# Optimization experiments

Measured on AMD Instinct MI355X. Metric: run time of the kernel, lower is better.

The kernel has to match this reference:

```python
import jax, jax.numpy as jnp
import numpy as np

NP_, NC_, E_, F_, D_, O_ = 50000, 100000, 600000, 69, 128, 2


def _embed(x, shift, scale, w1, b1, w2, b2):
    # PreNormLayer (shift+scale) -> Linear -> ReLU -> Linear -> ReLU
    x = (x + shift) * scale
    return jax.nn.relu(jax.nn.relu(x @ w1 + b1) @ w2 + b2)


def _biconv(left, src, dst, right, wl, bl, wr, sf, wf, bf, sp, wo1, bo1, wo2, bo2):
    # message: final( left_mod(right[dst]) + right_mod(left[src]) ), mean-scatter to dst
    pre = (right[dst] @ wl + bl) + left[src] @ wr            # [E, D]
    msg = jax.nn.relu(pre * sf) @ wf + bf                    # [E, D]
    n = right.shape[0]
    sums = jax.ops.segment_sum(msg, dst, num_segments=n)     # [N_right, D]
    cnt = jax.ops.segment_sum(jnp.ones((dst.shape[0], 1), msg.dtype), dst, num_segments=n)
    agg = sums / jnp.maximum(cnt, 1.0)
    h = jnp.concatenate([agg * sp, right], axis=-1)          # [N_right, 2D]
    return jax.nn.relu(h @ wo1 + bo1) @ wo2 + bo2


def setup_inputs():
    key = jax.random.key(0)
    ks = jax.random.split(key, 40)
    it = iter(range(4, 40))
    def nw(shape):
        return (jax.random.normal(ks[next(it)], shape, dtype=jnp.float32) * 0.05)
    inp = {}
    inp['pivot_features'] = jax.random.normal(ks[0], (NP_, F_), dtype=jnp.float32)
    inp['children_features'] = jax.random.normal(ks[1], (NC_, F_), dtype=jnp.float32)
    src = jax.random.randint(ks[2], (E_,), 0, NP_, dtype=jnp.int32)
    dst = jax.random.randint(ks[3], (E_,), 0, NC_, dtype=jnp.int32)
    inp['edge_indices'] = jnp.stack([src, dst], axis=0)
    # pivot / children embedding MLPs (PreNorm buffers at init values)
    for p in ('pe', 'ce'):
        inp[p + '_shift'] = jnp.zeros((F_,), jnp.float32)
        inp[p + '_scale'] = jnp.ones((F_,), jnp.float32)
        inp[p + '_w1'] = nw((F_, D_)); inp[p + '_b1'] = jnp.zeros((D_,), jnp.float32)
        inp[p + '_w2'] = nw((D_, D_)); inp[p + '_b2'] = jnp.zeros((D_,), jnp.float32)
    # two bipartite conv layers
    for p in ('vc', 'cv'):
        inp[p + '_wl'] = nw((D_, D_)); inp[p + '_bl'] = jnp.zeros((D_,), jnp.float32)
        inp[p + '_wr'] = nw((D_, D_))
        inp[p + '_sf'] = jnp.ones((1,), jnp.float32)   # PreNormLayer(1, shift=False) scale
        inp[p + '_wf'] = nw((D_, D_)); inp[p + '_bf'] = jnp.zeros((D_,), jnp.float32)
        inp[p + '_sp'] = jnp.ones((1,), jnp.float32)   # post_conv PreNormLayer scale
        inp[p + '_wo1'] = nw((2 * D_, D_)); inp[p + '_bo1'] = jnp.zeros((D_,), jnp.float32)
        inp[p + '_wo2'] = nw((D_, D_)); inp[p + '_bo2'] = jnp.zeros((D_,), jnp.float32)
    inp['out_w1'] = nw((D_, D_)); inp['out_b1'] = jnp.zeros((D_,), jnp.float32)
    inp['out_w2'] = nw((D_, O_)); inp['out_b2'] = jnp.zeros((O_,), jnp.float32)
    return inp


def reference(pivot_features, children_features, edge_indices,
              pe_shift, pe_scale, pe_w1, pe_b1, pe_w2, pe_b2,
              ce_shift, ce_scale, ce_w1, ce_b1, ce_w2, ce_b2,
              vc_wl, vc_bl, vc_wr, vc_sf, vc_wf, vc_bf, vc_sp, vc_wo1, vc_bo1, vc_wo2, vc_bo2,
              cv_wl, cv_bl, cv_wr, cv_sf, cv_wf, cv_bf, cv_sp, cv_wo1, cv_bo1, cv_wo2, cv_bo2,
              out_w1, out_b1, out_w2, out_b2):
    pv = _embed(pivot_features, pe_shift, pe_scale, pe_w1, pe_b1, pe_w2, pe_b2)
    ch = _embed(children_features, ce_shift, ce_scale, ce_w1, ce_b1, ce_w2, ce_b2)
    src, dst = edge_indices[0], edge_indices[1]
    # conv_v_to_c: left=pivot, right=children, aggregate to children
    ch = _biconv(pv, src, dst, ch, vc_wl, vc_bl, vc_wr, vc_sf, vc_wf, vc_bf, vc_sp,
                 vc_wo1, vc_bo1, vc_wo2, vc_bo2)
    # conv_c_to_v with reversed edges: left=children, right=pivot, aggregate to pivot
    pv = _biconv(ch, dst, src, pv, cv_wl, cv_bl, cv_wr, cv_sf, cv_wf, cv_bf, cv_sp,
                 cv_wo1, cv_bo1, cv_wo2, cv_bo2)
    return jax.nn.sigmoid(jax.nn.relu(pv @ out_w1 + out_b1) @ out_w2 + out_b2)
```

## Files before the change

### kernel.cpp

```cpp
#include <hip/hip_runtime.h>
#include <math.h>


typedef unsigned short u16;
typedef __attribute__((ext_vector_type(8))) short s8v;
typedef __attribute__((ext_vector_type(4))) float f4v;

__device__ __forceinline__ float bf2f(u16 u) {
    unsigned x = ((unsigned)u) << 16;
    return __builtin_bit_cast(float, x);
}
__device__ __forceinline__ u16 f2bf(float f) {
    unsigned x = __builtin_bit_cast(unsigned, f);
    unsigned r = x + 0x7fffu + ((x >> 16) & 1u);
    return (u16)(r >> 16);
}
__device__ __forceinline__ unsigned pk2(float a, float b) {
    return (unsigned)f2bf(a) | ((unsigned)f2bf(b) << 16);
}
__device__ __forceinline__ void unpack8(uint4 u, float* f) {
    f[0] = bf2f((u16)(u.x & 0xffff)); f[1] = bf2f((u16)(u.x >> 16));
    f[2] = bf2f((u16)(u.y & 0xffff)); f[3] = bf2f((u16)(u.y >> 16));
    f[4] = bf2f((u16)(u.z & 0xffff)); f[5] = bf2f((u16)(u.z >> 16));
    f[6] = bf2f((u16)(u.w & 0xffff)); f[7] = bf2f((u16)(u.w >> 16));
}

struct SmEnt { const float* A; const float* B; const float* s; };
struct SmPack { SmEnt e[4]; };

__global__ __launch_bounds__(256) void smallmm(SmPack p, float* __restrict__ out)
{
    int t = blockIdx.x * 256 + threadIdx.x;
    int m = t >> 14;
    int o = t & 16383;
    int i = o >> 7, j = o & 127;
    SmEnt en = p.e[m];
    float acc = 0.f;
#pragma unroll 4
    for (int k = 0; k < 128; ++k) acc += en.A[i * 128 + k] * en.B[k * 128 + j];
    if (en.s) acc *= *en.s;
    out[(size_t)m * 16384 + o] = acc;
}

__global__ void vecpre(
    const float* vc_bf, const float* vc_wo1, const float* vc_sp,
    const float* cv_bf, const float* cv_wo1, const float* cv_sp,
    const float* vc_bo2, const float* cv_wr,
    const float* cv_bo2, const float* out_w1, const float* out_b1,
    float* __restrict__ vout)
{
    int j = threadIdx.x;
    if (j >= 128) return;
    float a0 = 0.f, a1 = 0.f, a2 = 0.f, a3 = 0.f;
    for (int k = 0; k < 128; ++k) {
        a0 += vc_bf[k] * vc_wo1[k * 128 + j];
        a1 += cv_bf[k] * cv_wo1[k * 128 + j];
        a2 += vc_bo2[k] * cv_wr[k * 128 + j];
        a3 += cv_bo2[k] * out_w1[k * 128 + j];
    }
    vout[j] = a0 * (*vc_sp);
    vout[128 + j] = a1 * (*cv_sp);
    vout[256 + j] = a2;
    vout[384 + j] = a3 + out_b1[j];
}

struct WEnt { const float* src; int Ksrc; int Kdst; };
struct WPack { WEnt e[14]; };

__global__ __launch_bounds__(256) void wconvert(WPack p, u16* __restrict__ wt)
{
    int t = blockIdx.x * 256 + threadIdx.x;
    int m = t >> 15;
    int i = t & 32767;
    WEnt en = p.e[m];
    if (i >= (en.Kdst << 7)) return;
    int k = i >> 7, col = i & 127;
    float v = (k < en.Ksrc) ? en.src[k * 128 + col] : 0.f;
    wt[(size_t)m * 32768 + (size_t)col * en.Kdst + k] = f2bf(v);
}

__global__ __launch_bounds__(256) void featconv2(
    const float* __restrict__ pv, const float* __restrict__ ch,
    const float* __restrict__ psh, const float* __restrict__ psc,
    const float* __restrict__ csh, const float* __restrict__ csc,
    u16* __restrict__ y, long NPr, long total, int F)
{
    for (long i = (long)blockIdx.x * 256 + threadIdx.x; i < total;
         i += (long)gridDim.x * 256) {
        int cc = (int)(i % 96);
        long r = i / 96;
        const float *x, *sh, *sc;
        long row;
        if (r < NPr) { x = pv; sh = psh; sc = psc; row = r; }
        else { x = ch; sh = csh; sc = csc; row = r - NPr; }
        float v = 0.f;
        if (cc < F) {
            v = x[row * F + cc];
            v = (v + sh[cc]) * sc[cc];
        }
        y[i] = f2bf(v);
    }
}

template <int KS1, bool HASA2, bool RELU, bool GATE>
__global__ __launch_bounds__(256) void gemm_rb(
    const u16* __restrict__ A1, const u16* __restrict__ A2,
    const u16* __restrict__ WT1,
    const u16* __restrict__ WT2,
    const float* __restrict__ bias0,
    const float* __restrict__ bias1,
    const float* __restrict__ gate,
    u16* __restrict__ out, int M)
{
    constexpr int K1 = KS1 * 32;
    constexpr bool PF = !HASA2;
    constexpr int AS = KS1 + (HASA2 ? 4 : 0);
    const int lane = threadIdx.x & 63;
    const int c = lane & 15;
    const int kg = lane >> 4;
    const int wid = blockIdx.x * 4 + (threadIdx.x >> 6);
    const int ws = gridDim.x * 4;
    const int items = M >> 4;

    const u16* wbase = WT1 + (size_t)c * K1 + kg * 8;
    s8v bp[KS1][8];
#pragma unroll
    for (int ks = 0; ks < KS1; ++ks)
#pragma unroll
        for (int nt = 0; nt < 8; ++nt)
            bp[ks][nt] = *(const s8v*)(wbase + ((size_t)nt * 16) * K1 + ks * 32);

    const u16* wbase2 = HASA2 ? (WT2 + (size_t)c * 128 + kg * 8) : nullptr;

    f4v bq[8];
#pragma unroll
    for (int nt = 0; nt < 8; ++nt)
        bq[nt] = bias0 ? *(const f4v*)(bias0 + nt * 16 + kg * 4)
                       : (f4v){0.f, 0.f, 0.f, 0.f};

    auto lda = [&](s8v* a, int item) {
        const u16* ap = A1 + (size_t)((item << 4) + c) * K1 + kg * 8;
#pragma unroll
        for (int ks = 0; ks < KS1; ++ks) a[ks] = *(const s8v*)(ap + ks * 32);
        if (HASA2) {
            const u16* ap2 = A2 + (size_t)((item << 4) + c) * 128 + kg * 8;
#pragma unroll
            for (int ks = 0; ks < 4; ++ks) a[KS1 + ks] = *(const s8v*)(ap2 + ks * 32);
        }
    };

    s8v a[AS], an[AS], a2[AS];
    int item = wid;
    if (item < items) lda(a, item);
    if (PF && item + ws < items) lda(an, item + ws);
    while (item < items) {
        const int i2 = item + 2 * ws;
        if (PF && i2 < items) lda(a2, i2);

        f4v acc[8];
#pragma unroll
        for (int nt = 0; nt < 8; ++nt) acc[nt] = (f4v){0.f, 0.f, 0.f, 0.f};
#pragma unroll
        for (int ks = 0; ks < KS1; ++ks)
#pragma unroll
            for (int nt = 0; nt < 8; ++nt)
                acc[nt] = __builtin_amdgcn_mfma_f32_16x16x32_bf16(bp[ks][nt], a[ks], acc[nt], 0, 0, 0);
        if (HASA2) {
#pragma unroll
            for (int ks = 0; ks < 4; ++ks)
#pragma unroll
                for (int nt = 0; nt < 8; ++nt) {
                    s8v b = *(const s8v*)(wbase2 + ((size_t)nt * 16) * 128 + ks * 32);
                    acc[nt] = __builtin_amdgcn_mfma_f32_16x16x32_bf16(b, a[KS1 + ks], acc[nt], 0, 0, 0);
                }
        }

        const int r0 = item << 4;
        const float g = GATE ? (gate[r0 + c] > 0.f ? 1.f : 0.f) : 0.f;
        u16* op = out + (size_t)(r0 + c) * 128 + kg * 4;
#pragma unroll
        for (int nt = 0; nt < 8; ++nt) {
            float v0 = acc[nt][0] + bq[nt][0];
            float v1 = acc[nt][1] + bq[nt][1];
            float v2 = acc[nt][2] + bq[nt][2];
            float v3 = acc[nt][3] + bq[nt][3];
            if (GATE && bias1) {
                f4v b1q = *(const f4v*)(bias1 + nt * 16 + kg * 4);
                v0 += g * b1q[0]; v1 += g * b1q[1];
                v2 += g * b1q[2]; v3 += g * b1q[3];
            }
            if (RELU) {
                v0 = fmaxf(v0, 0.f); v1 = fmaxf(v1, 0.f);
                v2 = fmaxf(v2, 0.f); v3 = fmaxf(v3, 0.f);
            }
            uint2 pkv;
            pkv.x = pk2(v0, v1);
            pkv.y = pk2(v2, v3);
            *(uint2*)(op + nt * 16) = pkv;
        }

        if (PF) {
#pragma unroll
            for (int ks = 0; ks < AS; ++ks) { a[ks] = an[ks]; an[ks] = a2[ks]; }
        } else if (item + ws < items) {
            lda(a, item + ws);
        }
        item += ws;
    }
}

struct GJob { const u16* A1; const u16* WT1; const float* bias0; u16* out; int M; };
struct GJobs3 { GJob j[3]; };

template <int KS1, bool RELU>
__global__ __launch_bounds__(256) void gemm_multi(GJobs3 jobs)
{
    constexpr int K1 = KS1 * 32;
    const GJob jb = jobs.j[blockIdx.y];
    const u16* __restrict__ A1 = jb.A1;
    const float* __restrict__ bias0 = jb.bias0;
    u16* __restrict__ out = jb.out;
    const int lane = threadIdx.x & 63;
    const int c = lane & 15;
    const int kg = lane >> 4;
    const int wid = blockIdx.x * 4 + (threadIdx.x >> 6);
    const int ws = gridDim.x * 4;
    const int items = jb.M >> 4;

    const u16* wbase = jb.WT1 + (size_t)c * K1 + kg * 8;
    s8v bp[KS1][8];
#pragma unroll
    for (int ks = 0; ks < KS1; ++ks)
#pragma unroll
        for (int nt = 0; nt < 8; ++nt)
            bp[ks][nt] = *(const s8v*)(wbase + ((size_t)nt * 16) * K1 + ks * 32);

    f4v bq[8];
#pragma unroll
    for (int nt = 0; nt < 8; ++nt)
        bq[nt] = bias0 ? *(const f4v*)(bias0 + nt * 16 + kg * 4)
                       : (f4v){0.f, 0.f, 0.f, 0.f};

    auto lda = [&](s8v* a, int item) {
        const u16* ap = A1 + (size_t)((item << 4) + c) * K1 + kg * 8;
#pragma unroll
        for (int ks = 0; ks < KS1; ++ks) a[ks] = *(const s8v*)(ap + ks * 32);
    };

    s8v a[KS1], an[KS1], a2[KS1];
    int item = wid;
    if (item < items) lda(a, item);
    if (item + ws < items) lda(an, item + ws);
    while (item < items) {
        const int i2 = item + 2 * ws;
        if (i2 < items) lda(a2, i2);

        f4v acc[8];
#pragma unroll
        for (int nt = 0; nt < 8; ++nt) acc[nt] = (f4v){0.f, 0.f, 0.f, 0.f};
#pragma unroll
        for (int ks = 0; ks < KS1; ++ks)
#pragma unroll
            for (int nt = 0; nt < 8; ++nt)
                acc[nt] = __builtin_amdgcn_mfma_f32_16x16x32_bf16(bp[ks][nt], a[ks], acc[nt], 0, 0, 0);

        const int r0 = item << 4;
        u16* op = out + (size_t)(r0 + c) * 128 + kg * 4;
#pragma unroll
        for (int nt = 0; nt < 8; ++nt) {
            float v0 = acc[nt][0] + bq[nt][0];
            float v1 = acc[nt][1] + bq[nt][1];
            float v2 = acc[nt][2] + bq[nt][2];
            float v3 = acc[nt][3] + bq[nt][3];
            if (RELU) {
                v0 = fmaxf(v0, 0.f); v1 = fmaxf(v1, 0.f);
                v2 = fmaxf(v2, 0.f); v3 = fmaxf(v3, 0.f);
            }
            uint2 pkv;
            pkv.x = pk2(v0, v1);
            pkv.y = pk2(v2, v3);
            *(uint2*)(op + nt * 16) = pkv;
        }

#pragma unroll
        for (int ks = 0; ks < KS1; ++ks) { a[ks] = an[ks]; an[ks] = a2[ks]; }
        item += ws;
    }
}

__global__ __launch_bounds__(256) void head_fused(
    const u16* __restrict__ A1, const u16* __restrict__ WT,
    const float* __restrict__ b1, const float* __restrict__ w2,
    const float* __restrict__ b2, float* __restrict__ outp, int M)
{
    constexpr int KT = 128;
    const int lane = threadIdx.x & 63;
    const int c = lane & 15;
    const int kg = lane >> 4;
    const int wid = blockIdx.x * 4 + (threadIdx.x >> 6);
    const int ws = gridDim.x * 4;
    const int items = M >> 4;

    const u16* wbase = WT + (size_t)c * KT + kg * 8;
    s8v bp[4][8];
#pragma unroll
    for (int ks = 0; ks < 4; ++ks)
#pragma unroll
        for (int nt = 0; nt < 8; ++nt)
            bp[ks][nt] = *(const s8v*)(wbase + ((size_t)nt * 16) * KT + ks * 32);

    f4v bhq[8];
#pragma unroll
    for (int nt = 0; nt < 8; ++nt)
        bhq[nt] = *(const f4v*)(b1 + nt * 16 + kg * 4);
    const float s0 = b2[0], s1 = b2[1];

    for (int item = wid; item < items; item += ws) {
        const int r0 = item << 4;
        const u16* ap = A1 + (size_t)(r0 + c) * 128 + kg * 8;
        s8v a[4];
#pragma unroll
        for (int ks = 0; ks < 4; ++ks) a[ks] = *(const s8v*)(ap + ks * 32);

        f4v acc[8];
#pragma unroll
        for (int nt = 0; nt < 8; ++nt) acc[nt] = (f4v){0.f, 0.f, 0.f, 0.f};
#pragma unroll
        for (int ks = 0; ks < 4; ++ks)
#pragma unroll
            for (int nt = 0; nt < 8; ++nt)
                acc[nt] = __builtin_amdgcn_mfma_f32_16x16x32_bf16(bp[ks][nt], a[ks], acc[nt], 0, 0, 0);

        float p0 = 0.f, p1 = 0.f;
#pragma unroll
        for (int nt = 0; nt < 8; ++nt) {
            float v0 = fmaxf(acc[nt][0] + bhq[nt][0], 0.f);
            float v1 = fmaxf(acc[nt][1] + bhq[nt][1], 0.f);
            float v2 = fmaxf(acc[nt][2] + bhq[nt][2], 0.f);
            float v3 = fmaxf(acc[nt][3] + bhq[nt][3], 0.f);
            const float4 wa = *(const float4*)(w2 + (nt * 16 + kg * 4) * 2);
            const float4 wb = *(const float4*)(w2 + (nt * 16 + kg * 4) * 2 + 4);
            p0 += v0 * wa.x + v1 * wa.z + v2 * wb.x + v3 * wb.z;
            p1 += v0 * wa.y + v1 * wa.w + v2 * wb.y + v3 * wb.w;
        }
        p0 += __shfl_xor(p0, 16); p0 += __shfl_xor(p0, 32);
        p1 += __shfl_xor(p1, 16); p1 += __shfl_xor(p1, 32);
        if (kg == 0) {
            float2 o;
            o.x = 1.f / (1.f + expf(-(p0 + s0)));
            o.y = 1.f / (1.f + expf(-(p1 + s1)));
            *(float2*)(outp + (size_t)(r0 + c) * 2) = o;
        }
    }
}

__global__ __launch_bounds__(256) void binA(
    const int* __restrict__ src, const int* __restrict__ dst,
    int E, int CH, int NB, int nbk_c, int NBK,
    int* __restrict__ G, int* __restrict__ Tb)
{
    __shared__ int h[1024];
    const int blk = blockIdx.x, tid = threadIdx.x;
    for (int i = tid; i < NBK; i += 256) h[i] = 0;
    __syncthreads();
    const int e0 = blk * CH, e1 = min(E, e0 + CH);
    for (int e = e0 + tid; e < e1; e += 256) {
        atomicAdd(&h[dst[e] >> 9], 1);
        atomicAdd(&h[nbk_c + (src[e] >> 9)], 1);
    }
    __syncthreads();
    for (int b = tid; b < NBK; b += 256) {
        const int v = h[b];
        G[b * NB + blk] = v;
        if (v) atomicAdd(&Tb[b], v);
    }
}

__global__ __launch_bounds__(512) void binS(
    const int* __restrict__ Tb, int NBK, int* __restrict__ BB)
{
    __shared__ int wsum[8];
    const int tid = threadIdx.x;
    const int T = (tid < NBK) ? Tb[tid] : 0;
    const int lane = tid & 63, wv = tid >> 6;
    int incl = T;
#pragma unroll
    for (int d = 1; d < 64; d <<= 1) {
        int up = __shfl_up(incl, d);
        if (lane >= d) incl += up;
    }
    if (lane == 63) wsum[wv] = incl;
    __syncthreads();
    if (tid == 0) {
        int run = 0;
        for (int w = 0; w < 8; ++w) { int t = wsum[w]; wsum[w] = run; run += t; }
    }
    __syncthreads();
    const int base = wsum[wv] + incl - T;
    if (tid < NBK) {
        BB[tid] = base;
        if (tid == NBK - 1) BB[NBK] = base + T;
    }
}

__global__ __launch_bounds__(64) void binP(
    const int* __restrict__ G, const int* __restrict__ BB,
    int NB, int* __restrict__ PBB)
{
    const int b = blockIdx.x, l = threadIdx.x;
    const int* g = G + (size_t)b * NB;
    const int v0 = (l < NB) ? g[l] : 0;
    const int v1 = (l + 64 < NB) ? g[l + 64] : 0;
    int i0 = v0, i1 = v1;
#pragma unroll
    for (int d = 1; d < 64; d <<= 1) {
        int u0 = __shfl_up(i0, d);
        int u1 = __shfl_up(i1, d);
        if (l >= d) { i0 += u0; i1 += u1; }
    }
    const int t0 = __shfl(i0, 63);
    const int base = BB[b];
    int* p = PBB + (size_t)b * NB;
    if (l < NB) p[l] = base + i0 - v0;
    if (l + 64 < NB) p[l + 64] = base + t0 + i1 - v1;
}

__global__ __launch_bounds__(256) void binB(
    const int* __restrict__ src, const int* __restrict__ dst,
    int E, int CH, int NB, int nbk_c, int NBK,
    const int* __restrict__ PBB, unsigned* __restrict__ REC)
{
    __shared__ int fill[1024];
    const int blk = blockIdx.x, tid = threadIdx.x;
    for (int i = tid; i < NBK; i += 256) fill[i] = 0;
    __syncthreads();
    const int e0 = blk * CH, e1 = min(E, e0 + CH);
    for (int e = e0 + tid; e < e1; e += 256) {
        const int s = src[e], d = dst[e];
        const int bc = d >> 9;
        const int pc = PBB[bc * NB + blk] + atomicAdd(&fill[bc], 1);
        REC[pc] = (unsigned)s | ((unsigned)(d & 511) << 17);
        const int bp = nbk_c + (s >> 9);
        const int pp = PBB[bp * NB + blk] + atomicAdd(&fill[bp], 1);
        REC[pp] = (unsigned)d | ((unsigned)(s & 511) << 17);
    }
}

__global__ __launch_bounds__(256) void binC2(
    const unsigned* __restrict__ REC, const int* __restrict__ BB,
    int nbk_c, int NCn, int NPn,
    int* __restrict__ off_c, int* __restrict__ cnt_c,
    int* __restrict__ off_p, int* __restrict__ cnt_p, int* __restrict__ AJ)
{
    __shared__ int nh[512], lo[512], fl[512], ws2[4];
    const int b = blockIdx.x, tid = threadIdx.x;
    int Nn, node0;
    int *off_out, *cnt_out;
    if (b < nbk_c) { Nn = NCn; node0 = b << 9; off_out = off_c; cnt_out = cnt_c; }
    else { Nn = NPn; node0 = (b - nbk_c) << 9; off_out = off_p; cnt_out = cnt_p; }
    const int r0 = BB[b], r1 = BB[b + 1];
    const int kmax = min(512, Nn - node0);
    nh[tid] = 0; nh[tid + 256] = 0;
    fl[tid] = 0; fl[tid + 256] = 0;
    __syncthreads();
    for (int i = r0 + tid; i < r1; i += 256)
        atomicAdd(&nh[REC[i] >> 17], 1);
    __syncthreads();
    const int v0 = nh[2 * tid], v1 = nh[2 * tid + 1];
    const int s = v0 + v1;
    const int lane = tid & 63, wv = tid >> 6;
    int incl = s;
#pragma unroll
    for (int d = 1; d < 64; d <<= 1) {
        int up = __shfl_up(incl, d);
        if (lane >= d) incl += up;
    }
    if (lane == 63) ws2[wv] = incl;
    __syncthreads();
    if (tid == 0) {
        int run = 0;
        for (int w = 0; w < 4; ++w) { int t = ws2[w]; ws2[w] = run; run += t; }
    }
    __syncthreads();
    const int base = ws2[wv] + incl - s;
    lo[2 * tid] = base;
    lo[2 * tid + 1] = base + v0;
    __syncthreads();
    for (int k = tid; k < kmax; k += 256) {
        off_out[node0 + k] = r0 + lo[k];
        cnt_out[node0 + k] = nh[k];
    }
    for (int i = r0 + tid; i < r1; i += 256) {
        const unsigned rec = REC[i];
        const int k = rec >> 17;
        const int pos = r0 + lo[k] + atomicAdd(&fl[k], 1);
        AJ[pos] = (int)(rec & 0x1FFFFu);
    }
}

__global__ __launch_bounds__(256) void node_gather2(
    const int* __restrict__ off, const int* __restrict__ cnt,
    const int* __restrict__ adj,
    const u16* __restrict__ RW, const u16* __restrict__ LW,
    u16* __restrict__ Sdiv, float* __restrict__ cntf,
    const float* __restrict__ sf_p, int N)
{
    int t = blockIdx.x * 256 + threadIdx.x;
    int n = t >> 5;
    if (n >= N) return;
    int l32 = t & 31;
    int c = l32 & 15;
    int half = l32 >> 4;
    const float sf = *sf_p;
    const int start = off[n], len = cnt[n];

    float rw[8];
    unpack8(*(const uint4*)(RW + (size_t)n * 128 + c * 8), rw);
    float acc[8] = {0.f, 0.f, 0.f, 0.f, 0.f, 0.f, 0.f, 0.f};

    for (int i = half; i < len; i += 2) {
        int l = adj[start + i];
        float lw[8];
        unpack8(*(const uint4*)(LW + (size_t)l * 128 + c * 8), lw);
#pragma unroll
        for (int j = 0; j < 8; ++j)
            acc[j] += fmaxf((rw[j] + lw[j]) * sf, 0.f);
    }
#pragma unroll
    for (int j = 0; j < 8; ++j) acc[j] += __shfl_xor(acc[j], 16);

    if (half == 0) {
        float inv = 1.f / fmaxf((float)len, 1.f);
        uint4 o;
        o.x = pk2(acc[0] * inv, acc[1] * inv);
        o.y = pk2(acc[2] * inv, acc[3] * inv);
        o.z = pk2(acc[4] * inv, acc[5] * inv);
        o.w = pk2(acc[6] * inv, acc[7] * inv);
        *(uint4*)(Sdiv + (size_t)n * 128 + c * 8) = o;
        if (l32 == 0) cntf[n] = (float)len;
    }
}

extern "C" void kernel_launch(void* const* d_in, const int* in_sizes, int n_in,
                              void* d_out, int out_size, void* d_ws, size_t ws_size,
                              hipStream_t stream)
{
    const float* pivot = (const float*)d_in[0];
    const float* child = (const float*)d_in[1];
    const int* edges = (const int*)d_in[2];
    const int F = in_sizes[3];
    const int NP = in_sizes[0] / F;
    const int NC = in_sizes[1] / F;
    const int E = in_sizes[2] / 2;
    const int* src = edges;
    const int* dst = edges + E;

    const float *pe_shift = (const float*)d_in[3], *pe_scale = (const float*)d_in[4],
                *pe_w1 = (const float*)d_in[5], *pe_b1 = (const float*)d_in[6],
                *pe_w2 = (const float*)d_in[7], *pe_b2 = (const float*)d_in[8];
    const float *ce_shift = (const float*)d_in[9], *ce_scale = (const float*)d_in[10],
                *ce_w1 = (const float*)d_in[11], *ce_b1 = (const float*)d_in[12],
                *ce_w2 = (const float*)d_in[13], *ce_b2 = (const float*)d_in[14];
    const float *vc_wl = (const float*)d_in[15], *vc_bl = (const float*)d_in[16],
                *vc_wr = (const float*)d_in[17], *vc_sf = (const float*)d_in[18],
                *vc_wf = (const float*)d_in[19], *vc_bf = (const float*)d_in[20],
                *vc_sp = (const float*)d_in[21], *vc_wo1 = (const float*)d_in[22],
                *vc_bo1 = (const float*)d_in[23], *vc_wo2 = (const float*)d_in[24],
                *vc_bo2 = (const float*)d_in[25];
    const float *cv_wl = (const float*)d_in[26], *cv_bl = (const float*)d_in[27],
                *cv_wr = (const float*)d_in[28], *cv_sf = (const float*)d_in[29],
                *cv_wf = (const float*)d_in[30], *cv_bf = (const float*)d_in[31],
                *cv_sp = (const float*)d_in[32], *cv_wo1 = (const float*)d_in[33],
                *cv_bo1 = (const float*)d_in[34], *cv_wo2 = (const float*)d_in[35],
                *cv_bo2 = (const float*)d_in[36];
    const float *out_w1 = (const float*)d_in[37], *out_b1 = (const float*)d_in[38],
                *out_w2 = (const float*)d_in[39], *out_b2 = (const float*)d_in[40];

    char* base = (char*)d_ws;
    size_t off = 0;
    auto carve = [&](size_t bytes) {
        void* p = base + off;
        off += (bytes + 255) & ~(size_t)255;
        return p;
    };
    float* Wsc = (float*)carve((size_t)4 * 16384 * 4);
    float* Vsc = (float*)carve((size_t)4 * 128 * 4);
    u16* WT = (u16*)carve((size_t)14 * 32768 * 2);
    u16* FPC = (u16*)carve((size_t)(NP + NC) * 96 * 2);
    u16* FP = FPC;
    u16* FC = FPC + (size_t)NP * 96;
    u16* B0 = (u16*)carve((size_t)NP * 128 * 2);
    u16* B1 = (u16*)carve((size_t)NC * 128 * 2);
    u16* B2 = (u16*)carve((size_t)NC * 128 * 2);
    u16* B3 = (u16*)carve((size_t)NC * 128 * 2);
    u16* B4 = (u16*)carve((size_t)NC * 128 * 2);
    u16* B5 = (u16*)carve((size_t)NC * 128 * 2);
    u16* B6 = (u16*)carve((size_t)NP * 128 * 2);
    const int NMAX = (NC > NP) ? NC : NP;
    float* cntf = (float*)carve((size_t)NMAX * 4);

    const int NB = 120;
    const int CH = (E + NB - 1) / NB;
    const int nbk_c = (NC + 511) >> 9;
    const int nbk_p = (NP + 511) >> 9;
    const int NBK = nbk_c + nbk_p;
    int* cnt_c = (int*)carve((size_t)NC * 4);
    int* cnt_p = (int*)carve((size_t)NP * 4);
    int* off_c = (int*)carve((size_t)NC * 4);
    int* off_p = (int*)carve((size_t)NP * 4);
    int* G = (int*)carve((size_t)NBK * NB * 4);
    int* PBB = (int*)carve((size_t)NBK * NB * 4);
    int* BB = (int*)carve((size_t)(NBK + 1) * 4);
    int* Tb = (int*)carve((size_t)NBK * 4);
    unsigned* REC = (unsigned*)carve((size_t)2 * E * 4);
    int* AJ = (int*)carve((size_t)2 * E * 4);

    SmPack sp;
    sp.e[0] = {vc_wf, vc_wo1, vc_sp};
    sp.e[1] = {cv_wf, cv_wo1, cv_sp};
    sp.e[2] = {vc_wo2, cv_wr, nullptr};
    sp.e[3] = {cv_wo2, out_w1, nullptr};
    hipLaunchKernelGGL(smallmm, dim3(256), dim3(256), 0, stream, sp, Wsc);
    hipLaunchKernelGGL(vecpre, dim3(1), dim3(128), 0, stream,
                       vc_bf, vc_wo1, vc_sp, cv_bf, cv_wo1, cv_sp,
                       vc_bo2, cv_wr, cv_bo2, out_w1, out_b1, Vsc);
    const float* cvec_vc = Vsc;
    const float* cvec_cv = Vsc + 128;
    const float* cx = Vsc + 256;
    const float* bh = Vsc + 384;

    WPack wp;
    auto setw = [&](int i, const float* s, int ks, int kd) {
        wp.e[i].src = s; wp.e[i].Ksrc = ks; wp.e[i].Kdst = kd;
    };
    setw(0, pe_w1, F, 96);            setw(1, pe_w2, 128, 128);
    setw(2, ce_w1, F, 96);            setw(3, ce_w2, 128, 128);
    setw(4, vc_wl, 128, 128);         setw(5, vc_wr, 128, 128);
    setw(6, Wsc + 0 * 16384, 128, 128);
    setw(7, vc_wo1 + 128 * 128, 128, 128);
    setw(8, Wsc + 2 * 16384, 128, 128);
    setw(9, cv_wl, 128, 128);         setw(10, cv_wr, 128, 128);
    setw(11, Wsc + 1 * 16384, 128, 128);
    setw(12, cv_wo1 + 128 * 128, 128, 128);
    setw(13, Wsc + 3 * 16384, 128, 128);
    hipLaunchKernelGGL(wconvert, dim3(14 * 128), dim3(256), 0, stream, wp, WT);
    auto wt = [&](int i) { return WT + (size_t)i * 32768; };

    hipLaunchKernelGGL(featconv2, dim3(2048), dim3(256), 0, stream,
                       pivot, child, pe_shift, pe_scale, ce_shift, ce_scale,
                       FPC, (long)NP, (long)(NP + NC) * 96, F);

    hipMemsetAsync(Tb, 0, (size_t)NBK * 4, stream);
    hipLaunchKernelGGL(binA, dim3(NB), dim3(256), 0, stream,
                       src, dst, E, CH, NB, nbk_c, NBK, G, Tb);
    hipLaunchKernelGGL(binS, dim3(1), dim3(512), 0, stream, Tb, NBK, BB);
    hipLaunchKernelGGL(binP, dim3(NBK), dim3(64), 0, stream, G, BB, NB, PBB);
    hipLaunchKernelGGL(binB, dim3(NB), dim3(256), 0, stream,
                       src, dst, E, CH, NB, nbk_c, NBK, PBB, REC);
    hipLaunchKernelGGL(binC2, dim3(NBK), dim3(256), 0, stream,
                       REC, BB, nbk_c, NC, NP, off_c, cnt_c, off_p, cnt_p, AJ);

    const dim3 blk(256);
    auto grd = [](int M) {
        int items = M >> 4;
        int b = (items + 3) / 4;
        return dim3((unsigned)(b < 512 ? b : 512));
    };

    {
        GJobs3 j;
        j.j[0] = {FP, wt(0), pe_b1, B1, NP};
        j.j[1] = {FC, wt(2), ce_b1, B5, NC};
        j.j[2] = j.j[0];
        dim3 g = grd(NC); g.y = 2;
        hipLaunchKernelGGL(HIP_KERNEL_NAME(gemm_multi<3, true>), g, blk, 0, stream, j);
    }
    {
        GJobs3 j;
        j.j[0] = {B1, wt(1), pe_b2, B0, NP};
        j.j[1] = {B5, wt(3), ce_b2, B2, NC};
        j.j[2] = j.j[0];
        dim3 g = grd(NC); g.y = 2;
        hipLaunchKernelGGL(HIP_KERNEL_NAME(gemm_multi<4, true>), g, blk, 0, stream, j);
    }
    {
        GJobs3 j;
        j.j[0] = {B2, wt(4), vc_bl, B1, NC};
        j.j[1] = {B0, wt(5), nullptr, B3, NP};
        j.j[2] = {B0, wt(9), cv_bl, B6, NP};
        dim3 g = grd(NC); g.y = 3;
        hipLaunchKernelGGL(HIP_KERNEL_NAME(gemm_multi<4, false>), g, blk, 0, stream, j);
    }

    hipLaunchKernelGGL(node_gather2, dim3(((size_t)NC * 32 + 255) / 256), blk, 0,
                       stream, off_c, cnt_c, AJ, B1, B3, B4, cntf, vc_sf, NC);
    gemm_rb<4, true, true, true><<<grd(NC), blk, 0, stream>>>(
        B4, B2, wt(6), wt(7), vc_bo1, cvec_vc, cntf, B5, NC);
    gemm_rb<4, false, false, false><<<grd(NC), blk, 0, stream>>>(
        B5, nullptr, wt(8), nullptr, cx, nullptr, nullptr, B3, NC);

    hipLaunchKernelGGL(node_gather2, dim3(((size_t)NP * 32 + 255) / 256), blk, 0,
                       stream, off_p, cnt_p, AJ, B6, B3, B4, cntf, cv_sf, NP);
    gemm_rb<4, true, true, true><<<grd(NP), blk, 0, stream>>>(
        B4, B0, wt(11), wt(12), cv_bo1, cvec_cv, cntf, B1, NP);

    hipLaunchKernelGGL(head_fused, grd(NP), blk, 0, stream,
                       B1, wt(13), bh, out_w2, out_b2, (float*)d_out, NP);
}
```

Measured before the change: 373.7 us.

## Fuse two-layer embedding MLPs into one kernel and drop batched multi-GEMM launches

```diff
diff --git a/kernel.cpp b/kernel.cpp
--- a/kernel.cpp
+++ b/kernel.cpp
@@ -99,6 +99,103 @@
             v = (v + sh[cc]) * sc[cc];
         }
         y[i] = f2bf(v);
+    }
+}
+
+__global__ __launch_bounds__(256) void embed_fused(
+    const u16* __restrict__ A, const u16* __restrict__ W1,
+    const float* __restrict__ b1, const u16* __restrict__ W2,
+    const float* __restrict__ b2, u16* __restrict__ out, int M)
+{
+    __shared__ u16 w2s[128 * 136];
+    __shared__ u16 tile[4][16 * 136];
+    const int tid = threadIdx.x;
+    for (int i = tid; i < 8192; i += 256) {
+        int col = i >> 6, kp = (i & 63) << 1;
+        *(unsigned*)&w2s[col * 136 + kp] = *(const unsigned*)&W2[(size_t)col * 128 + kp];
+    }
+    __syncthreads();
+
+    const int lane = tid & 63;
+    const int c = lane & 15;
+    const int kg = lane >> 4;
+    const int wv = tid >> 6;
+    const int wid = blockIdx.x * 4 + wv;
+    const int ws = gridDim.x * 4;
+    const int items = M >> 4;
+    u16* tl = tile[wv];
+
+    const u16* wbase = W1 + (size_t)c * 96 + kg * 8;
+    s8v bp1[3][8];
+#pragma unroll
+    for (int ks = 0; ks < 3; ++ks)
+#pragma unroll
+        for (int nt = 0; nt < 8; ++nt)
+            bp1[ks][nt] = *(const s8v*)(wbase + ((size_t)nt * 16) * 96 + ks * 32);
+
+    f4v b1q[8], b2q[8];
+#pragma unroll
+    for (int nt = 0; nt < 8; ++nt) {
+        b1q[nt] = *(const f4v*)(b1 + nt * 16 + kg * 4);
+        b2q[nt] = *(const f4v*)(b2 + nt * 16 + kg * 4);
+    }
+
+    for (int item = wid; item < items; item += ws) {
+        const int r0 = item << 4;
+        const u16* ap = A + (size_t)(r0 + c) * 96 + kg * 8;
+        s8v a[3];
+#pragma unroll
+        for (int ks = 0; ks < 3; ++ks) a[ks] = *(const s8v*)(ap + ks * 32);
+
+        f4v acc[8];
+#pragma unroll
+        for (int nt = 0; nt < 8; ++nt) acc[nt] = (f4v){0.f, 0.f, 0.f, 0.f};
+#pragma unroll
+        for (int ks = 0; ks < 3; ++ks)
+#pragma unroll
+            for (int nt = 0; nt < 8; ++nt)
+                acc[nt] = __builtin_amdgcn_mfma_f32_16x16x32_bf16(bp1[ks][nt], a[ks], acc[nt], 0, 0, 0);
+
+#pragma unroll
+        for (int nt = 0; nt < 8; ++nt) {
+            float v0 = fmaxf(acc[nt][0] + b1q[nt][0], 0.f);
+            float v1 = fmaxf(acc[nt][1] + b1q[nt][1], 0.f);
+            float v2 = fmaxf(acc[nt][2] + b1q[nt][2], 0.f);
+            float v3 = fmaxf(acc[nt][3] + b1q[nt][3], 0.f);
+            uint2 pkv;
+            pkv.x = pk2(v0, v1);
+            pkv.y = pk2(v2, v3);
+            *(uint2*)&tl[c * 136 + nt * 16 + kg * 4] = pkv;
+        }
+
+        s8v a2[4];
+#pragma unroll
+        for (int ks = 0; ks < 4; ++ks)
+            a2[ks] = *(const s8v*)&tl[c * 136 + ks * 32 + kg * 8];
+
+        f4v acc2[8];
+#pragma unroll
+        for (int nt = 0; nt < 8; ++nt) acc2[nt] = (f4v){0.f, 0.f, 0.f, 0.f};
+#pragma unroll
+        for (int ks = 0; ks < 4; ++ks)
+#pragma unroll
+            for (int nt = 0; nt < 8; ++nt) {
+                s8v b = *(const s8v*)&w2s[(size_t)(nt * 16 + c) * 136 + ks * 32 + kg * 8];
+                acc2[nt] = __builtin_amdgcn_mfma_f32_16x16x32_bf16(b, a2[ks], acc2[nt], 0, 0, 0);
+            }
+
+        u16* op = out + (size_t)(r0 + c) * 128 + kg * 4;
+#pragma unroll
+        for (int nt = 0; nt < 8; ++nt) {
+            float v0 = fmaxf(acc2[nt][0] + b2q[nt][0], 0.f);
+            float v1 = fmaxf(acc2[nt][1] + b2q[nt][1], 0.f);
+            float v2 = fmaxf(acc2[nt][2] + b2q[nt][2], 0.f);
+            float v3 = fmaxf(acc2[nt][3] + b2q[nt][3], 0.f);
+            uint2 pkv;
+            pkv.x = pk2(v0, v1);
+            pkv.y = pk2(v2, v3);
+            *(uint2*)(op + nt * 16) = pkv;
+        }
     }
 }
 
@@ -205,85 +302,6 @@
         } else if (item + ws < items) {
             lda(a, item + ws);
         }
-        item += ws;
-    }
-}
-
-struct GJob { const u16* A1; const u16* WT1; const float* bias0; u16* out; int M; };
-struct GJobs3 { GJob j[3]; };
-
-template <int KS1, bool RELU>
-__global__ __launch_bounds__(256) void gemm_multi(GJobs3 jobs)
-{
-    constexpr int K1 = KS1 * 32;
-    const GJob jb = jobs.j[blockIdx.y];
-    const u16* __restrict__ A1 = jb.A1;
-    const float* __restrict__ bias0 = jb.bias0;
-    u16* __restrict__ out = jb.out;
-    const int lane = threadIdx.x & 63;
-    const int c = lane & 15;
-    const int kg = lane >> 4;
-    const int wid = blockIdx.x * 4 + (threadIdx.x >> 6);
-    const int ws = gridDim.x * 4;
-    const int items = jb.M >> 4;
-
-    const u16* wbase = jb.WT1 + (size_t)c * K1 + kg * 8;
-    s8v bp[KS1][8];
-#pragma unroll
-    for (int ks = 0; ks < KS1; ++ks)
-#pragma unroll
-        for (int nt = 0; nt < 8; ++nt)
-            bp[ks][nt] = *(const s8v*)(wbase + ((size_t)nt * 16) * K1 + ks * 32);
-
-    f4v bq[8];
-#pragma unroll
-    for (int nt = 0; nt < 8; ++nt)
-        bq[nt] = bias0 ? *(const f4v*)(bias0 + nt * 16 + kg * 4)
-                       : (f4v){0.f, 0.f, 0.f, 0.f};
-
-    auto lda = [&](s8v* a, int item) {
-        const u16* ap = A1 + (size_t)((item << 4) + c) * K1 + kg * 8;
-#pragma unroll
-        for (int ks = 0; ks < KS1; ++ks) a[ks] = *(const s8v*)(ap + ks * 32);
-    };
-
-    s8v a[KS1], an[KS1], a2[KS1];
-    int item = wid;
-    if (item < items) lda(a, item);
-    if (item + ws < items) lda(an, item + ws);
-    while (item < items) {
-        const int i2 = item + 2 * ws;
-        if (i2 < items) lda(a2, i2);
-
-        f4v acc[8];
-#pragma unroll
-        for (int nt = 0; nt < 8; ++nt) acc[nt] = (f4v){0.f, 0.f, 0.f, 0.f};
-#pragma unroll
-        for (int ks = 0; ks < KS1; ++ks)
-#pragma unroll
-            for (int nt = 0; nt < 8; ++nt)
-                acc[nt] = __builtin_amdgcn_mfma_f32_16x16x32_bf16(bp[ks][nt], a[ks], acc[nt], 0, 0, 0);
-
-        const int r0 = item << 4;
-        u16* op = out + (size_t)(r0 + c) * 128 + kg * 4;
-#pragma unroll
-        for (int nt = 0; nt < 8; ++nt) {
-            float v0 = acc[nt][0] + bq[nt][0];
-            float v1 = acc[nt][1] + bq[nt][1];
-            float v2 = acc[nt][2] + bq[nt][2];
-            float v3 = acc[nt][3] + bq[nt][3];
-            if (RELU) {
-                v0 = fmaxf(v0, 0.f); v1 = fmaxf(v1, 0.f);
-                v2 = fmaxf(v2, 0.f); v3 = fmaxf(v3, 0.f);
-            }
-            uint2 pkv;
-            pkv.x = pk2(v0, v1);
-            pkv.y = pk2(v2, v3);
-            *(uint2*)(op + nt * 16) = pkv;
-        }
-
-#pragma unroll
-        for (int ks = 0; ks < KS1; ++ks) { a[ks] = an[ks]; an[ks] = a2[ks]; }
         item += ws;
     }
 }
@@ -667,30 +685,17 @@
         return dim3((unsigned)(b < 512 ? b : 512));
     };
 
-    {
-        GJobs3 j;
-        j.j[0] = {FP, wt(0), pe_b1, B1, NP};
-        j.j[1] = {FC, wt(2), ce_b1, B5, NC};
-        j.j[2] = j.j[0];
-        dim3 g = grd(NC); g.y = 2;
-        hipLaunchKernelGGL(HIP_KERNEL_NAME(gemm_multi<3, true>), g, blk, 0, stream, j);
-    }
-    {
-        GJobs3 j;
-        j.j[0] = {B1, wt(1), pe_b2, B0, NP};
-        j.j[1] = {B5, wt(3), ce_b2, B2, NC};
-        j.j[2] = j.j[0];
-        dim3 g = grd(NC); g.y = 2;
-        hipLaunchKernelGGL(HIP_KERNEL_NAME(gemm_multi<4, true>), g, blk, 0, stream, j);
-    }
-    {
-        GJobs3 j;
-        j.j[0] = {B2, wt(4), vc_bl, B1, NC};
-        j.j[1] = {B0, wt(5), nullptr, B3, NP};
-        j.j[2] = {B0, wt(9), cv_bl, B6, NP};
-        dim3 g = grd(NC); g.y = 3;
-        hipLaunchKernelGGL(HIP_KERNEL_NAME(gemm_multi<4, false>), g, blk, 0, stream, j);
-    }
+    hipLaunchKernelGGL(embed_fused, grd(NP), blk, 0, stream,
+                       FP, wt(0), pe_b1, wt(1), pe_b2, B0, NP);
+    hipLaunchKernelGGL(embed_fused, grd(NC), blk, 0, stream,
+                       FC, wt(2), ce_b1, wt(3), ce_b2, B2, NC);
+
+    gemm_rb<4, false, false, false><<<grd(NC), blk, 0, stream>>>(
+        B2, nullptr, wt(4), nullptr, vc_bl, nullptr, nullptr, B1, NC);
+    gemm_rb<4, false, false, false><<<grd(NP), blk, 0, stream>>>(
+        B0, nullptr, wt(5), nullptr, nullptr, nullptr, nullptr, B3, NP);
+    gemm_rb<4, false, false, false><<<grd(NP), blk, 0, stream>>>(
+        B0, nullptr, wt(9), nullptr, cv_bl, nullptr, nullptr, B6, NP);
 
     hipLaunchKernelGGL(node_gather2, dim3(((size_t)NC * 32 + 255) / 256), blk, 0,
                        stream, off_c, cnt_c, AJ, B1, B3, B4, cntf, vc_sf, NC);
```

Result: no change. 379.3 us (+1.5%).
